# Kernel tuning notes

Hardware: AMD Instinct MI355X
Metric: run time of the kernel (lower is better)

## Reference

```python
import jax, jax.numpy as jnp
import numpy as np

IP = 10  # power-iteration steps


def setup_inputs() -> dict:
    key = jax.random.key(0)
    k1, k2 = jax.random.split(key)
    B, C, H, W = 16, 512, 64, 64
    x = jax.random.normal(k1, (B, C, H, W), dtype=jnp.float32)
    # random start vector for power iteration (torch: FloatTensor.normal_(0,1))
    v = jax.random.normal(k2, (B, C, 1), dtype=jnp.float32)
    return {"x": x, "v": v}


def reference(x, v):
    B, C, H, W = x.shape
    # w = x.view(B,C,HW).permute(0,2,1) -> (B, HW, C)
    w = jnp.transpose(x.reshape(B, C, H * W), (0, 2, 1))
    # W_s = w^T w : (B, C, C)
    Ws = jnp.einsum('bnc,bnd->bcd', w, w)

    def step(vc, _):
        vc = jnp.matmul(Ws, vc)                                   # (B,C,1)
        vc = vc / jnp.linalg.norm(vc, axis=(1, 2), keepdims=True)  # per-batch L2 norm
        return vc, None

    v, _ = jax.lax.scan(step, v, None, length=IP)
    # u = W v, normalized : (B, HW, 1)
    u = jnp.matmul(w, v)
    u = u / jnp.linalg.norm(u, axis=(1, 2), keepdims=True)
    # z = u v^T : (B, HW, C) -> (B, C, H, W)
    z = jnp.matmul(u, jnp.transpose(v, (0, 2, 1)))
    z = jnp.transpose(z, (0, 2, 1)).reshape(B, C, H, W)
    return x + z
```

## Files before the change

kernel.cpp:

```cpp
#include <hip/hip_runtime.h>
#include <stdint.h>

#define NB 16
#define NC 512
#define NHW 4096

typedef unsigned short u16;
typedef __bf16 bf16x8 __attribute__((ext_vector_type(8)));
typedef float f32x4 __attribute__((ext_vector_type(4)));
typedef unsigned short u16x8 __attribute__((ext_vector_type(8)));
typedef unsigned short u16x4 __attribute__((ext_vector_type(4)));

#define AS1 __attribute__((address_space(1)))
#define AS3 __attribute__((address_space(3)))

__device__ __forceinline__ float bf2f(u16 h) {
    union { unsigned u; float f; } a; a.u = ((unsigned)h) << 16; return a.f;
}
__device__ __forceinline__ u16 f2bf(float f) {
    union { float f; unsigned u; } a; a.f = f;
    unsigned u = a.u;
    return (u16)((u + 0x7FFFu + ((u >> 16) & 1u)) >> 16);
}

__global__ __launch_bounds__(256) void k_to_bf16(const float* __restrict__ x,
                                                 u16* __restrict__ xb) {
    int i = blockIdx.x * 256 + threadIdx.x;
    f32x4 v = ((const f32x4*)x)[i];
    u16x4 o;
    o[0] = f2bf(v[0]); o[1] = f2bf(v[1]); o[2] = f2bf(v[2]); o[3] = f2bf(v[3]);
    ((u16x4*)xb)[i] = o;
}

__global__ __launch_bounds__(256, 2)
void k_gemm_bt(const u16* __restrict__ Ab, const u16* __restrict__ Bb,
               u16* __restrict__ Cb, int K, int N,
               size_t sA, size_t sB, size_t sC, float scale) {
    __shared__ u16 As[128 * 32];
    __shared__ u16 Bs[128 * 32];
    const int tid = threadIdx.x;
    const int wave = tid >> 6, lane = tid & 63;
    const int b = blockIdx.z;
    const u16* A  = Ab + (size_t)b * sA + (size_t)blockIdx.x * 128 * K;
    const u16* Bm = Bb + (size_t)b * sB + (size_t)blockIdx.y * 128 * K;

    const int srow = tid >> 2;
    const int scol = (tid & 3) * 8;
    const u16* ag0 = A  + (size_t)srow * K + scol;
    const u16* ag1 = ag0 + (size_t)64 * K;
    const u16* bg0 = Bm + (size_t)srow * K + scol;
    const u16* bg1 = bg0 + (size_t)64 * K;
    u16* asw0 = &As[wave * 512];
    u16* asw1 = &As[2048 + wave * 512];
    u16* bsw0 = &Bs[wave * 512];
    u16* bsw1 = &Bs[2048 + wave * 512];

    f32x4 acc[4][4];
#pragma unroll
    for (int i = 0; i < 4; i++)
#pragma unroll
        for (int j = 0; j < 4; j++) acc[i][j] = f32x4{0.f, 0.f, 0.f, 0.f};

    const int rm = (wave & 1) * 64;
    const int rn = (wave >> 1) * 64;
    const int m16 = lane & 15, quad = lane >> 4;

    for (int k0 = 0; k0 < K; k0 += 32) {
        __syncthreads();
        __builtin_amdgcn_global_load_lds((AS1 void*)(ag0 + k0), (AS3 void*)asw0, 16, 0, 0);
        __builtin_amdgcn_global_load_lds((AS1 void*)(ag1 + k0), (AS3 void*)asw1, 16, 0, 0);
        __builtin_amdgcn_global_load_lds((AS1 void*)(bg0 + k0), (AS3 void*)bsw0, 16, 0, 0);
        __builtin_amdgcn_global_load_lds((AS1 void*)(bg1 + k0), (AS3 void*)bsw1, 16, 0, 0);
        __syncthreads();

        bf16x8 af[4], bfr[4];
#pragma unroll
        for (int mi = 0; mi < 4; mi++)
            af[mi] = *(const bf16x8*)&As[(rm + mi * 16 + m16) * 32 + quad * 8];
#pragma unroll
        for (int ni = 0; ni < 4; ni++)
            bfr[ni] = *(const bf16x8*)&Bs[(rn + ni * 16 + m16) * 32 + quad * 8];
#pragma unroll
        for (int mi = 0; mi < 4; mi++)
#pragma unroll
            for (int ni = 0; ni < 4; ni++)
                acc[mi][ni] = __builtin_amdgcn_mfma_f32_16x16x32_bf16(
                    af[mi], bfr[ni], acc[mi][ni], 0, 0, 0);
    }

    u16* Co = Cb + (size_t)b * sC + ((size_t)blockIdx.x * 128) * N + blockIdx.y * 128;
    const int rq = quad * 4;
#pragma unroll
    for (int mi = 0; mi < 4; mi++)
#pragma unroll
        for (int ni = 0; ni < 4; ni++)
#pragma unroll
            for (int r = 0; r < 4; r++) {
                int row = rm + mi * 16 + rq + r;
                int col = rn + ni * 16 + m16;
                Co[(size_t)row * N + col] = f2bf(acc[mi][ni][r] * scale);
            }
}

__global__ __launch_bounds__(1024, 1)
void k_power_iter(const u16* __restrict__ S2, const float* __restrict__ v0,
                  float* __restrict__ vhat) {
    const int b = blockIdx.x, tid = threadIdx.x;
    __shared__ float va[NC], vb[NC];
    __shared__ float part[NC][16];
    __shared__ float red[16];
    const u16* Mb = S2 + (size_t)b * NC * NC;
    const int cg = tid & 15;
    const int r0 = tid >> 4;
    if (tid < NC) va[tid] = v0[b * NC + tid];
    float* cur = va;
    float* nxt = vb;
    __syncthreads();

    for (int it = 0; it < 5; ++it) {
        float c[4][8];
#pragma unroll
        for (int p = 0; p < 4; p++) {
            f32x4 lo = *(const f32x4*)&cur[cg * 8 + p * 128];
            f32x4 hi = *(const f32x4*)&cur[cg * 8 + p * 128 + 4];
            c[p][0] = lo[0]; c[p][1] = lo[1]; c[p][2] = lo[2]; c[p][3] = lo[3];
            c[p][4] = hi[0]; c[p][5] = hi[1]; c[p][6] = hi[2]; c[p][7] = hi[3];
        }
#pragma unroll 2
        for (int pass = 0; pass < 8; ++pass) {
            const int r = pass * 64 + r0;
            const u16* row = Mb + (size_t)r * NC + cg * 8;
            u16x8 m[4];
#pragma unroll
            for (int p = 0; p < 4; p++) m[p] = *(const u16x8*)(row + p * 128);
            float a0 = 0.f, a1 = 0.f, a2 = 0.f, a3 = 0.f;
#pragma unroll
            for (int j = 0; j < 8; j++) {
                a0 += bf2f(m[0][j]) * c[0][j];
                a1 += bf2f(m[1][j]) * c[1][j];
                a2 += bf2f(m[2][j]) * c[2][j];
                a3 += bf2f(m[3][j]) * c[3][j];
            }
            part[r][cg] = (a0 + a1) + (a2 + a3);
        }
        __syncthreads();
        if (tid < NC) {
            f32x4 s0 = *(const f32x4*)&part[tid][0];
            f32x4 s1 = *(const f32x4*)&part[tid][4];
            f32x4 s2 = *(const f32x4*)&part[tid][8];
            f32x4 s3 = *(const f32x4*)&part[tid][12];
            f32x4 s = (s0 + s1) + (s2 + s3);
            nxt[tid] = (s[0] + s[1]) + (s[2] + s[3]);
        }
        __syncthreads();
        float* t = cur; cur = nxt; nxt = t;
    }

    float mv = (tid < NC) ? cur[tid] : 0.f;
    float x = mv * mv;
#pragma unroll
    for (int o = 32; o > 0; o >>= 1) x += __shfl_down(x, o, 64);
    if ((tid & 63) == 0) red[tid >> 6] = x;
    __syncthreads();
    float n = red[0];
#pragma unroll
    for (int w = 1; w < 16; w++) n += red[w];
    if (tid < NC) vhat[b * NC + tid] = mv * rsqrtf(n);
}

__global__ __launch_bounds__(256)
void k_compute_t(const u16* __restrict__ xb, const float* __restrict__ vhat,
                 float* __restrict__ tp) {
    const int b = blockIdx.z, cc = blockIdx.y, nc = blockIdx.x, tid = threadIdx.x;
    __shared__ float vsh[128];
    if (tid < 128) vsh[tid] = vhat[b * NC + cc * 128 + tid];
    __syncthreads();
    const int n0 = nc * 2048 + tid * 8;
    const u16* xp = xb + (size_t)b * NC * NHW + (size_t)cc * 128 * NHW + n0;
    float acc[8] = {0.f, 0.f, 0.f, 0.f, 0.f, 0.f, 0.f, 0.f};
    for (int c = 0; c < 128; c++) {
        u16x8 w = *(const u16x8*)xp;
        xp += NHW;
        float vc = vsh[c];
#pragma unroll
        for (int j = 0; j < 8; j++) acc[j] += bf2f(w[j]) * vc;
    }
    float* dst = tp + (size_t)(b * 4 + cc) * NHW + n0;
    *(f32x4*)dst       = f32x4{acc[0], acc[1], acc[2], acc[3]};
    *(f32x4*)(dst + 4) = f32x4{acc[4], acc[5], acc[6], acc[7]};
}

__global__ __launch_bounds__(1024, 1)
void k_tnorm(const float* __restrict__ tp, float* __restrict__ tsum,
             float* __restrict__ sinv) {
    const int b = blockIdx.x, tid = threadIdx.x;
    __shared__ float red[16];
    const int n0 = tid * 4;
    f32x4 s = f32x4{0.f, 0.f, 0.f, 0.f};
#pragma unroll
    for (int p = 0; p < 4; p++)
        s += *(const f32x4*)(tp + (size_t)(b * 4 + p) * NHW + n0);
    *(f32x4*)(tsum + (size_t)b * NHW + n0) = s;
    float ss = s[0] * s[0] + s[1] * s[1] + s[2] * s[2] + s[3] * s[3];
#pragma unroll
    for (int o = 32; o > 0; o >>= 1) ss += __shfl_down(ss, o, 64);
    if ((tid & 63) == 0) red[tid >> 6] = ss;
    __syncthreads();
    if (tid == 0) {
        float n = red[0];
#pragma unroll
        for (int w = 1; w < 16; w++) n += red[w];
        sinv[b] = rsqrtf(n);
    }
}

__global__ __launch_bounds__(256)
void k_epilogue(const float* __restrict__ x, const float* __restrict__ tsum,
                const float* __restrict__ vhat, const float* __restrict__ sinv,
                float* __restrict__ out) {
    const int b = blockIdx.z, cc = blockIdx.y, nc = blockIdx.x, tid = threadIdx.x;
    __shared__ float tl[1024];
    __shared__ float cf[64];
    const int nbase = nc * 1024, cbase = cc * 64;
    const float si = sinv[b];
    for (int i = tid; i < 1024; i += 256)
        tl[i] = tsum[(size_t)b * NHW + nbase + i];
    if (tid < 64) cf[tid] = vhat[b * NC + cbase + tid] * si;
    __syncthreads();
    f32x4 tv = ((const f32x4*)tl)[tid];
    for (int rr = 0; rr < 64; rr++) {
        size_t off = ((size_t)(b * NC + cbase + rr)) * NHW + nbase + tid * 4;
        f32x4 xv = *(const f32x4*)(x + off);
        float c = cf[rr];
        f32x4 o = xv + tv * c;
        *(f32x4*)(out + off) = o;
    }
}

extern "C" void kernel_launch(void* const* d_in, const int* in_sizes, int n_in,
                              void* d_out, int out_size, void* d_ws, size_t ws_size,
                              hipStream_t stream) {
    const float* x  = (const float*)d_in[0];
    const float* v0 = (const float*)d_in[1];
    float* out = (float*)d_out;

    char* ws = (char*)d_ws;
    u16* xb     = (u16*)ws;
    u16* S      = (u16*)(ws + 67108864);
    u16* S2     = (u16*)(ws + 67108864 + 8388608);
    float* vhat = (float*)(ws + 83886080);
    float* tp   = (float*)(ws + 83886080 + 65536);
    float* tsum = (float*)(ws + 83886080 + 65536 + 1048576);
    float* sinv = (float*)(ws + 83886080 + 65536 + 1048576 + 262144);

    k_to_bf16<<<dim3(32768), dim3(256), 0, stream>>>(x, xb);
    k_gemm_bt<<<dim3(4, 4, NB), dim3(256), 0, stream>>>(
        xb, xb, S, NHW, NC, (size_t)NC * NHW, (size_t)NC * NHW, (size_t)NC * NC,
        1.f / 4096.f);
    k_gemm_bt<<<dim3(4, 4, NB), dim3(256), 0, stream>>>(
        S, S, S2, NC, NC, (size_t)NC * NC, (size_t)NC * NC, (size_t)NC * NC, 1.f);
    k_power_iter<<<dim3(NB), dim3(1024), 0, stream>>>(S2, v0, vhat);
    k_compute_t<<<dim3(2, 4, NB), dim3(256), 0, stream>>>(xb, vhat, tp);
    k_tnorm<<<dim3(NB), dim3(1024), 0, stream>>>(tp, tsum, sinv);
    k_epilogue<<<dim3(4, 8, NB), dim3(256), 0, stream>>>(x, tsum, vhat, sinv, out);
}
```

Baseline: 402.6 us.

## Double-buffer LDS in batched GEMM and shrink M tile for more blocks

The batched bf16 GEMM now uses two LDS buffers so the next K-slice loads while the current one feeds the MFMAs, which cuts a barrier per step. The M tile drops from 128 to 64 rows and the grid doubles to 512 blocks, since 256 blocks underfill the GPU's compute units. Each wave now computes a 64x32 tile instead of 64x64, which lowers arithmetic intensity and re-reads the B tile more often.

```diff
diff --git a/kernel.cpp b/kernel.cpp
--- a/kernel.cpp
+++ b/kernel.cpp
@@ -36,70 +36,85 @@
 void k_gemm_bt(const u16* __restrict__ Ab, const u16* __restrict__ Bb,
                u16* __restrict__ Cb, int K, int N,
                size_t sA, size_t sB, size_t sC, float scale) {
-    __shared__ u16 As[128 * 32];
-    __shared__ u16 Bs[128 * 32];
+    __shared__ u16 As[2][64 * 32];
+    __shared__ u16 Bs[2][128 * 32];
     const int tid = threadIdx.x;
     const int wave = tid >> 6, lane = tid & 63;
     const int b = blockIdx.z;
-    const u16* A  = Ab + (size_t)b * sA + (size_t)blockIdx.x * 128 * K;
+    const u16* A  = Ab + (size_t)b * sA + (size_t)blockIdx.x * 64 * K;
     const u16* Bm = Bb + (size_t)b * sB + (size_t)blockIdx.y * 128 * K;
 
     const int srow = tid >> 2;
     const int scol = (tid & 3) * 8;
     const u16* ag0 = A  + (size_t)srow * K + scol;
-    const u16* ag1 = ag0 + (size_t)64 * K;
     const u16* bg0 = Bm + (size_t)srow * K + scol;
     const u16* bg1 = bg0 + (size_t)64 * K;
-    u16* asw0 = &As[wave * 512];
-    u16* asw1 = &As[2048 + wave * 512];
-    u16* bsw0 = &Bs[wave * 512];
-    u16* bsw1 = &Bs[2048 + wave * 512];
-
-    f32x4 acc[4][4];
+
+#define STAGE(BUF, KO)                                                         \
+    {                                                                          \
+        __builtin_amdgcn_global_load_lds((AS1 void*)(ag0 + (KO)),              \
+            (AS3 void*)(&As[BUF][wave * 512]), 16, 0, 0);                      \
+        __builtin_amdgcn_global_load_lds((AS1 void*)(bg0 + (KO)),              \
+            (AS3 void*)(&Bs[BUF][wave * 512]), 16, 0, 0);                      \
+        __builtin_amdgcn_global_load_lds((AS1 void*)(bg1 + (KO)),              \
+            (AS3 void*)(&Bs[BUF][2048 + wave * 512]), 16, 0, 0);               \
+    }
+
+    f32x4 acc[4][2];
 #pragma unroll
     for (int i = 0; i < 4; i++)
 #pragma unroll
-        for (int j = 0; j < 4; j++) acc[i][j] = f32x4{0.f, 0.f, 0.f, 0.f};
-
-    const int rm = (wave & 1) * 64;
-    const int rn = (wave >> 1) * 64;
+        for (int j = 0; j < 2; j++) acc[i][j] = f32x4{0.f, 0.f, 0.f, 0.f};
+
+    const int cn = wave * 32;
     const int m16 = lane & 15, quad = lane >> 4;
 
-    for (int k0 = 0; k0 < K; k0 += 32) {
-        __syncthreads();
-        __builtin_amdgcn_global_load_lds((AS1 void*)(ag0 + k0), (AS3 void*)asw0, 16, 0, 0);
-        __builtin_amdgcn_global_load_lds((AS1 void*)(ag1 + k0), (AS3 void*)asw1, 16, 0, 0);
-        __builtin_amdgcn_global_load_lds((AS1 void*)(bg0 + k0), (AS3 void*)bsw0, 16, 0, 0);
-        __builtin_amdgcn_global_load_lds((AS1 void*)(bg1 + k0), (AS3 void*)bsw1, 16, 0, 0);
-        __syncthreads();
-
-        bf16x8 af[4], bfr[4];
-#pragma unroll
-        for (int mi = 0; mi < 4; mi++)
-            af[mi] = *(const bf16x8*)&As[(rm + mi * 16 + m16) * 32 + quad * 8];
-#pragma unroll
-        for (int ni = 0; ni < 4; ni++)
-            bfr[ni] = *(const bf16x8*)&Bs[(rn + ni * 16 + m16) * 32 + quad * 8];
-#pragma unroll
-        for (int mi = 0; mi < 4; mi++)
-#pragma unroll
-            for (int ni = 0; ni < 4; ni++)
-                acc[mi][ni] = __builtin_amdgcn_mfma_f32_16x16x32_bf16(
-                    af[mi], bfr[ni], acc[mi][ni], 0, 0, 0);
-    }
-
-    u16* Co = Cb + (size_t)b * sC + ((size_t)blockIdx.x * 128) * N + blockIdx.y * 128;
+#define COMPUTE(BUF)                                                           \
+    {                                                                          \
+        bf16x8 af[4], bfr[2];                                                  \
+        _Pragma("unroll")                                                      \
+        for (int mi = 0; mi < 4; mi++)                                         \
+            af[mi] = *(const bf16x8*)&As[BUF][(mi * 16 + m16) * 32 +           \
+                                             quad * 8];                        \
+        _Pragma("unroll")                                                      \
+        for (int ni = 0; ni < 2; ni++)                                         \
+            bfr[ni] = *(const bf16x8*)&Bs[BUF][(cn + ni * 16 + m16) * 32 +     \
+                                              quad * 8];                       \
+        _Pragma("unroll")                                                      \
+        for (int mi = 0; mi < 4; mi++)                                         \
+            _Pragma("unroll")                                                  \
+            for (int ni = 0; ni < 2; ni++)                                     \
+                acc[mi][ni] = __builtin_amdgcn_mfma_f32_16x16x32_bf16(         \
+                    af[mi], bfr[ni], acc[mi][ni], 0, 0, 0);                    \
+    }
+
+    STAGE(0, 0);
+    __syncthreads();
+
+    for (int k0 = 0; k0 < K; k0 += 64) {
+        STAGE(1, k0 + 32);
+        COMPUTE(0);
+        __syncthreads();
+        if (k0 + 64 < K) STAGE(0, k0 + 64);
+        COMPUTE(1);
+        __syncthreads();
+    }
+
+    u16* Co = Cb + (size_t)b * sC + ((size_t)blockIdx.x * 64) * N +
+              (size_t)blockIdx.y * 128;
     const int rq = quad * 4;
 #pragma unroll
     for (int mi = 0; mi < 4; mi++)
 #pragma unroll
-        for (int ni = 0; ni < 4; ni++)
+        for (int ni = 0; ni < 2; ni++)
 #pragma unroll
             for (int r = 0; r < 4; r++) {
-                int row = rm + mi * 16 + rq + r;
-                int col = rn + ni * 16 + m16;
+                int row = mi * 16 + rq + r;
+                int col = cn + ni * 16 + m16;
                 Co[(size_t)row * N + col] = f2bf(acc[mi][ni][r] * scale);
             }
+#undef STAGE
+#undef COMPUTE
 }
 
 __global__ __launch_bounds__(1024, 1)
@@ -254,11 +269,12 @@
     float* sinv = (float*)(ws + 83886080 + 65536 + 1048576 + 262144);
 
     k_to_bf16<<<dim3(32768), dim3(256), 0, stream>>>(x, xb);
-    k_gemm_bt<<<dim3(4, 4, NB), dim3(256), 0, stream>>>(
+    k_gemm_bt<<<dim3(8, 4, NB), dim3(256), 0, stream>>>(
         xb, xb, S, NHW, NC, (size_t)NC * NHW, (size_t)NC * NHW, (size_t)NC * NC,
         1.f / 4096.f);
-    k_gemm_bt<<<dim3(4, 4, NB), dim3(256), 0, stream>>>(
-        S, S, S2, NC, NC, (size_t)NC * NC, (size_t)NC * NC, (size_t)NC * NC, 1.f);
+    k_gemm_bt<<<dim3(8, 4, NB), dim3(256), 0, stream>>>(
+        S, S, S2, NC, NC, (size_t)NC * NC, (size_t)NC * NC, (size_t)NC * NC,
+        1.f);
     k_power_iter<<<dim3(NB), dim3(1024), 0, stream>>>(S2, v0, vhat);
     k_compute_t<<<dim3(2, 4, NB), dim3(256), 0, stream>>>(xb, vhat, tp);
     k_tnorm<<<dim3(NB), dim3(1024), 0, stream>>>(tp, tsum, sinv);
```

Result: slower. 410.8 us (+2.0%).
